# Performance work log

Measured on AMD Instinct MI355X. Metric: run time of the kernel, lower is better.

The kernel has to match this reference:

```python
import jax, jax.numpy as jnp
import numpy as np

N_HEAD = 16

def setup_inputs() -> dict:
    key = jax.random.key(0)
    ks = jax.random.split(key, 5)
    d = 1024
    x = jax.random.normal(ks[0], (2, 2048, d), dtype=jnp.float32)
    Wqkv = jax.random.normal(ks[1], (d, 3 * d), dtype=jnp.float32) * (1.0 / np.sqrt(d))
    bqkv = jnp.zeros((3 * d,), dtype=jnp.float32)
    Wproj = jax.random.normal(ks[2], (d, d), dtype=jnp.float32) * (1.0 / np.sqrt(d))
    bproj = jnp.zeros((d,), dtype=jnp.float32)
    return {"x": x, "Wqkv": Wqkv, "bqkv": bqkv, "Wproj": Wproj, "bproj": bproj}


def reference(x, Wqkv, bqkv, Wproj, bproj):
    B, T, C = x.shape
    H = N_HEAD
    Dh = C // H
    qkv = x @ Wqkv + bqkv                      # [B, T, 3C]
    q, k, v = jnp.split(qkv, 3, axis=-1)
    # [B, T, C] -> [B, H, T, Dh]
    q = q.reshape(B, T, H, Dh).transpose(0, 2, 1, 3)
    k = k.reshape(B, T, H, Dh).transpose(0, 2, 1, 3)
    v = v.reshape(B, T, H, Dh).transpose(0, 2, 1, 3)
    scale = 1.0 / np.sqrt(Dh)
    att = jnp.einsum('bhqd,bhkd->bhqk', q, k) * scale
    causal = jnp.tril(jnp.ones((T, T), dtype=bool))
    att = jnp.where(causal[None, None, :, :], att, jnp.float32(-jnp.inf))
    att = jax.nn.softmax(att, axis=-1)
    y = jnp.einsum('bhqk,bhkd->bhqd', att, v)  # [B, H, T, Dh]
    y = y.transpose(0, 2, 1, 3).reshape(B, T, C)
    return y @ Wproj + bproj
```

## Files before the change

kernel.cpp:

```cpp
#include <hip/hip_runtime.h>
#include <math.h>


typedef __attribute__((ext_vector_type(8))) short short8;
typedef __attribute__((ext_vector_type(4))) short short4v;
typedef __attribute__((ext_vector_type(4))) float floatx4;
typedef __attribute__((ext_vector_type(16))) float floatx16;
typedef __attribute__((ext_vector_type(2))) unsigned int uint2v;
typedef __attribute__((ext_vector_type(4))) unsigned int uint4v;

__device__ __forceinline__ unsigned short f2bf(float f) {
  unsigned u = __float_as_uint(f);
  return (unsigned short)((u + 0x7fff + ((u >> 16) & 1)) >> 16);
}

__device__ __forceinline__ unsigned cvtpk(float a, float b) {
  unsigned r;
  asm("v_cvt_pk_bf16_f32 %0, %1, %2" : "=v"(r) : "v"(a), "v"(b));
  return r;
}

__device__ __forceinline__ short8 mk8(unsigned w0, unsigned w1, unsigned w2,
                                      unsigned w3) {
  uint4v v = {w0, w1, w2, w3};
  return __builtin_bit_cast(short8, v);
}

__device__ __forceinline__ void gld16(const unsigned short* g, unsigned short* l) {
  __builtin_amdgcn_global_load_lds(
      (const __attribute__((address_space(1))) unsigned int*)g,
      (__attribute__((address_space(3))) unsigned int*)l, 16, 0, 0);
}

__device__ __forceinline__ void vmcnt4() {
  asm volatile("s_waitcnt vmcnt(4)" ::: "memory");
}
__device__ __forceinline__ void vmcnt0() {
  asm volatile("s_waitcnt vmcnt(0)" ::: "memory");
}

__device__ __forceinline__ void pack_a_body(const float* __restrict__ in,
                                            unsigned short* __restrict__ out,
                                            int K, int m0, int k0,
                                            unsigned short (*lds)[72], int t) {
  {
    int ml = t >> 2, kl = (t & 3) * 16;
    const float4* p = (const float4*)(in + (size_t)(m0 + ml) * K + k0 + kl);
    unsigned short* q = &lds[ml][kl];
#pragma unroll
    for (int c = 0; c < 4; ++c) {
      float4 v = p[c];
      q[c * 4 + 0] = f2bf(v.x);
      q[c * 4 + 1] = f2bf(v.y);
      q[c * 4 + 2] = f2bf(v.z);
      q[c * 4 + 3] = f2bf(v.w);
    }
  }
  __syncthreads();
  int chunk = t >> 3, sub = t & 7;
  int mt = chunk >> 3, kc = chunk & 7;
  unsigned short tmp[16];
#pragma unroll
  for (int j2 = 0; j2 < 2; ++j2)
#pragma unroll
    for (int j = 0; j < 8; ++j)
      tmp[j2 * 8 + j] = lds[mt * 16 + sub * 2 + j2][kc * 8 + j];
  size_t ofs = ((size_t)(m0 >> 4) + mt) * (16 * (size_t)K) +
               ((size_t)(k0 >> 3) + kc) * 128 + sub * 16;
  *(int4*)(out + ofs) = *(int4*)(tmp);
  *(int4*)(out + ofs + 8) = *(int4*)(tmp + 8);
}

__device__ __forceinline__ void pack_bt_body(const float* __restrict__ in,
                                             unsigned short* __restrict__ out,
                                             int K, int N, int n0, int k0,
                                             unsigned short (*lds)[72], int t) {
  {
    int kl = t >> 2, nl = (t & 3) * 16;
    const float4* p = (const float4*)(in + (size_t)(k0 + kl) * N + n0 + nl);
#pragma unroll
    for (int c = 0; c < 4; ++c) {
      float4 v = p[c];
      lds[nl + c * 4 + 0][kl] = f2bf(v.x);
      lds[nl + c * 4 + 1][kl] = f2bf(v.y);
      lds[nl + c * 4 + 2][kl] = f2bf(v.z);
      lds[nl + c * 4 + 3][kl] = f2bf(v.w);
    }
  }
  __syncthreads();
  int chunk = t >> 3, sub = t & 7;
  int nt = chunk >> 3, kc = chunk & 7;
  unsigned short tmp[16];
#pragma unroll
  for (int j2 = 0; j2 < 2; ++j2)
#pragma unroll
    for (int j = 0; j < 8; ++j)
      tmp[j2 * 8 + j] = lds[nt * 16 + sub * 2 + j2][kc * 8 + j];
  size_t ofs = ((size_t)(n0 >> 4) + nt) * (16 * (size_t)K) +
               ((size_t)(k0 >> 3) + kc) * 128 + sub * 16;
  *(int4*)(out + ofs) = *(int4*)(tmp);
  *(int4*)(out + ofs + 8) = *(int4*)(tmp + 8);
}

__global__ __launch_bounds__(256) void pack_all(
    const float* __restrict__ x, const float* __restrict__ Wqkv,
    const float* __restrict__ Wproj, unsigned short* __restrict__ xbf,
    unsigned short* __restrict__ wqkvF, unsigned short* __restrict__ wprojF) {
  __shared__ __align__(16) unsigned short lds[64][72];
  const int b = blockIdx.x, t = threadIdx.x;
  if (b < 1024) {
    pack_a_body(x, xbf, 1024, (b >> 4) * 64, (b & 15) * 64, lds, t);
  } else if (b < 1792) {
    int b2 = b - 1024;
    pack_bt_body(Wqkv, wqkvF, 1024, 3072, (b2 % 48) * 64, (b2 / 48) * 64, lds, t);
  } else {
    int b3 = b - 1792;
    pack_bt_body(Wproj, wprojF, 1024, 1024, (b3 & 15) * 64, (b3 >> 4) * 64, lds, t);
  }
}

template <int MODE>
__global__ __launch_bounds__(256, 3) void gemm_lds(
    const unsigned short* __restrict__ A, const unsigned short* __restrict__ B,
    const float* __restrict__ bias, float* __restrict__ Cout,
    unsigned short* __restrict__ Qb, unsigned short* __restrict__ Kb,
    unsigned short* __restrict__ Vt, int M, int N, int K) {
  const int tid = threadIdx.x;
  const int wave = tid >> 6, lane = tid & 63;
  const int quad = lane >> 4, l15 = lane & 15;
  const int wr = wave >> 1, wc = wave & 1;

  const int nbn = N >> 7;
  const int colsPerX = nbn >> 3;
  const int xcd = (int)(blockIdx.x & 7);
  const int idx = (int)(blockIdx.x >> 3);
  const int bn = xcd * colsPerX + (colsPerX == 1 ? 0 : (idx % colsPerX));
  const int bm = (colsPerX == 1) ? idx : (idx / colsPerX);

  const int mt0 = bm * 8;
  const int nt0 = bn * 8;

  __shared__ __align__(16) unsigned short As[8192];
  __shared__ __align__(16) unsigned short Bs[8192];

  const unsigned short* spA[4];
  const unsigned short* spB[4];
#pragma unroll
  for (int j = 0; j < 4; ++j) {
    int c = wave * 4 + j;
    spA[j] = A + ((size_t)(mt0 + (c >> 1))) * (16 * (size_t)K) +
             (c & 1) * 512 + lane * 8;
    spB[j] = B + ((size_t)(nt0 + (c >> 1))) * (16 * (size_t)K) +
             (c & 1) * 512 + lane * 8;
  }

  floatx4 acc[4][4];
#pragma unroll
  for (int i = 0; i < 4; ++i)
#pragma unroll
    for (int j = 0; j < 4; ++j) acc[i][j] = (floatx4)0.0f;

  const int fofs = quad * 128 + l15 * 8;
  const int nk = K >> 6;

  for (int kk = 0; kk < nk; ++kk) {
#pragma unroll
    for (int j = 0; j < 4; ++j) {
      gld16(spA[j], &As[(wave * 4 + j) * 512]);
      gld16(spB[j], &Bs[(wave * 4 + j) * 512]);
      spA[j] += 1024;
      spB[j] += 1024;
    }
    __syncthreads();

#pragma unroll
    for (int ks = 0; ks < 2; ++ks) {
      short8 fa[4], fb[4];
#pragma unroll
      for (int im = 0; im < 4; ++im)
        fa[im] = *(const short8*)&As[((wr * 4 + im) * 2 + ks) * 512 + fofs];
#pragma unroll
      for (int in = 0; in < 4; ++in)
        fb[in] = *(const short8*)&Bs[((wc * 4 + in) * 2 + ks) * 512 + fofs];
#pragma unroll
      for (int im = 0; im < 4; ++im)
#pragma unroll
        for (int in = 0; in < 4; ++in)
          acc[im][in] = __builtin_amdgcn_mfma_f32_16x16x32_bf16(
              fa[im], fb[in], acc[im][in], 0, 0, 0);
    }
    if (kk + 1 < nk) __syncthreads();
  }

  const int m0w = bm * 128 + wr * 64;
  const int n0w = bn * 128 + wc * 64;

  if (MODE == 0) {
    const float QSCALE = 0.18033688f;
#pragma unroll
    for (int im = 0; im < 4; ++im) {
      int mbase = m0w + im * 16 + quad * 4;
      int bb = mbase >> 11, tb = mbase & 2047;
#pragma unroll
      for (int in = 0; in < 4; ++in) {
        int n = n0w + in * 16 + l15;
        float bv = bias[n];
        int which = n >> 10;
        int h = (n >> 6) & 15;
        int d = n & 63;
        size_t bh_ = (size_t)(bb * 16 + h);
        if (which == 2) {
          size_t base = bh_ * 131072 + (size_t)(d >> 5) * 65536 +
                        (size_t)(tb >> 4) * 512 +
                        (size_t)((d & 31) + 32 * ((tb & 15) >> 3)) * 8 +
                        (tb & 7);
          short4v pk;
#pragma unroll
          for (int r = 0; r < 4; ++r) pk[r] = (short)f2bf(acc[im][in][r] + bv);
          *(short4v*)(Vt + base) = pk;
        } else {
          size_t base = bh_ * 131072 + (size_t)(tb >> 5) * 2048 +
                        (size_t)(d >> 4) * 512 +
                        (size_t)((tb & 31) + 32 * ((d & 15) >> 3)) * 8 +
                        (d & 7);
          if (which == 0) {
#pragma unroll
            for (int r = 0; r < 4; ++r)
              Qb[base + r * 8] = f2bf((acc[im][in][r] + bv) * QSCALE);
          } else {
#pragma unroll
            for (int r = 0; r < 4; ++r)
              Kb[base + r * 8] = f2bf(acc[im][in][r] + bv);
          }
        }
      }
    }
  } else {
#pragma unroll
    for (int im = 0; im < 4; ++im) {
      int mbase = m0w + im * 16 + quad * 4;
#pragma unroll
      for (int in = 0; in < 4; ++in) {
        int n = n0w + in * 16 + l15;
        float bv = bias[n];
#pragma unroll
        for (int r = 0; r < 4; ++r)
          Cout[(size_t)(mbase + r) * N + n] = acc[im][in][r] + bv;
      }
    }
  }
}

__device__ __forceinline__ void pack_swap(const floatx16& s, short8& lo,
                                          short8& hi) {
  unsigned P0 = cvtpk(s[0], s[1]), P1 = cvtpk(s[2], s[3]);
  unsigned P2 = cvtpk(s[4], s[5]), P3 = cvtpk(s[6], s[7]);
  unsigned P4 = cvtpk(s[8], s[9]), P5 = cvtpk(s[10], s[11]);
  unsigned P6 = cvtpk(s[12], s[13]), P7 = cvtpk(s[14], s[15]);
  uint2v a = __builtin_amdgcn_permlane32_swap(P0, P2, false, false);
  uint2v b = __builtin_amdgcn_permlane32_swap(P1, P3, false, false);
  uint2v c = __builtin_amdgcn_permlane32_swap(P4, P6, false, false);
  uint2v d = __builtin_amdgcn_permlane32_swap(P5, P7, false, false);
  lo = mk8(a.x, b.x, a.y, b.y);
  hi = mk8(c.x, d.x, c.y, d.y);
}

__global__ __launch_bounds__(256, 2) void attn_mfma(
    const unsigned short* __restrict__ Q, const unsigned short* __restrict__ K,
    const unsigned short* __restrict__ Vt, unsigned short* __restrict__ Y) {
  const int b = (int)blockIdx.x;
  const int xcd = b & 7, qi = b >> 3;
  const int bh = xcd * 4 + (qi & 3);
  const int m = 15 - (qi >> 2);
  const int wave = threadIdx.x >> 6;
  const int lane = threadIdx.x & 63;
  const int j = m * 4 + wave;
  const int t0 = j * 32;
  const int l31 = lane & 31, h = lane >> 5;
  const int lofs8 = lane * 8;

  __shared__ __align__(16) unsigned short KV[2][8192];

  const unsigned short* Qb = Q + (size_t)bh * 131072;
  const unsigned short* Kb = K + (size_t)bh * 131072;
  const unsigned short* Vb = Vt + (size_t)bh * 131072;

  auto stage = [&](int buf, int jtN) {
    unsigned short* l = &KV[buf][wave * 2048];
    const unsigned short* g =
        (wave < 2) ? (Kb + (size_t)jtN * 4096 + wave * 2048)
                   : (Vb + (size_t)(wave & 1) * 65536 + (size_t)jtN * 2048);
    g += lofs8;
#pragma unroll
    for (int i = 0; i < 4; ++i) gld16(g + i * 512, l + i * 512);
  };

  short8 qf[4];
#pragma unroll
  for (int c = 0; c < 4; ++c)
    qf[c] = *(const short8*)(Qb + (size_t)j * 2048 + c * 512 + lofs8);

  floatx16 o0 = (floatx16)0.0f, o1 = (floatx16)0.0f;
  float lp[4] = {0.f, 0.f, 0.f, 0.f};

  const int ntiles = (j >> 1) + 1;
  const int ntB = 2 * m + 2;

  stage(0, 0);
  int cur = 0;

  for (int jt = 0; jt < ntB; ++jt) {
    if (jt + 1 < ntB) {
      stage(cur ^ 1, jt + 1);
      vmcnt4();
    } else {
      vmcnt0();
    }
    __builtin_amdgcn_s_barrier();
    __builtin_amdgcn_sched_barrier(0);

    const unsigned short* Lb = KV[cur];
    short8 kf0[4], kf1[4];
#pragma unroll
    for (int c = 0; c < 4; ++c) {
      kf0[c] = *(const short8*)&Lb[c * 512 + lofs8];
      kf1[c] = *(const short8*)&Lb[2048 + c * 512 + lofs8];
    }

    floatx16 sa0 = (floatx16)0.0f, sa1 = (floatx16)0.0f;
#pragma unroll
    for (int c = 0; c < 4; ++c) {
      sa0 = __builtin_amdgcn_mfma_f32_32x32x16_bf16(kf0[c], qf[c], sa0, 0, 0, 0);
      sa1 = __builtin_amdgcn_mfma_f32_32x32x16_bf16(kf1[c], qf[c], sa1, 0, 0, 0);
    }

    if (jt >= ntiles - 1) {
#pragma unroll
      for (int r = 0; r < 16; ++r) {
        int row = (r & 3) + 8 * (r >> 2) + 4 * h;
        int key = jt * 64 + row;
        if (key > t0 + l31) sa0[r] = -__builtin_inff();
        if (key + 32 > t0 + l31) sa1[r] = -__builtin_inff();
      }
    }

#pragma unroll
    for (int r = 0; r < 16; ++r) {
      float p0 = exp2f(sa0[r]);
      float p1 = exp2f(sa1[r]);
      sa0[r] = p0;
      sa1[r] = p1;
      lp[r & 3] += p0 + p1;
    }

    short8 pb0, pb1, pb2, pb3;
    pack_swap(sa0, pb0, pb1);
    pack_swap(sa1, pb2, pb3);

    short8 vf0[4], vf1[4];
#pragma unroll
    for (int kc = 0; kc < 4; ++kc) {
      vf0[kc] = *(const short8*)&Lb[4096 + kc * 512 + lofs8];
      vf1[kc] = *(const short8*)&Lb[6144 + kc * 512 + lofs8];
    }

    o0 = __builtin_amdgcn_mfma_f32_32x32x16_bf16(vf0[0], pb0, o0, 0, 0, 0);
    o1 = __builtin_amdgcn_mfma_f32_32x32x16_bf16(vf1[0], pb0, o1, 0, 0, 0);
    o0 = __builtin_amdgcn_mfma_f32_32x32x16_bf16(vf0[1], pb1, o0, 0, 0, 0);
    o1 = __builtin_amdgcn_mfma_f32_32x32x16_bf16(vf1[1], pb1, o1, 0, 0, 0);
    o0 = __builtin_amdgcn_mfma_f32_32x32x16_bf16(vf0[2], pb2, o0, 0, 0, 0);
    o1 = __builtin_amdgcn_mfma_f32_32x32x16_bf16(vf1[2], pb2, o1, 0, 0, 0);
    o0 = __builtin_amdgcn_mfma_f32_32x32x16_bf16(vf0[3], pb3, o0, 0, 0, 0);
    o1 = __builtin_amdgcn_mfma_f32_32x32x16_bf16(vf1[3], pb3, o1, 0, 0, 0);

    __builtin_amdgcn_sched_barrier(0);
    __builtin_amdgcn_s_barrier();
    cur ^= 1;
  }

  float l_acc = (lp[0] + lp[1]) + (lp[2] + lp[3]);
  l_acc += __shfl_xor(l_acc, 32);
  const float inv = 1.0f / l_acc;

  const int b_ = bh >> 4, hh = bh & 15;
  const int mglob = b_ * 2048 + t0 + l31;
  const size_t mofs = (size_t)(mglob >> 4) * 16384 + (size_t)(mglob & 15) * 8;
#pragma unroll
  for (int db = 0; db < 2; ++db) {
    const floatx16& o = db ? o1 : o0;
#pragma unroll
    for (int g = 0; g < 4; ++g) {
      int d0 = db * 32 + 8 * g + 4 * h;
      int kf0 = hh * 64 + d0;
      size_t ofs = mofs + (size_t)(kf0 >> 3) * 128 + (kf0 & 7);
      short4v pk;
#pragma unroll
      for (int r = 0; r < 4; ++r) pk[r] = (short)f2bf(o[4 * g + r] * inv);
      *(short4v*)(Y + ofs) = pk;
    }
  }
}

extern "C" void kernel_launch(void* const* d_in, const int* in_sizes, int n_in,
                              void* d_out, int out_size, void* d_ws,
                              size_t ws_size, hipStream_t stream) {
  const float* x = (const float*)d_in[0];
  const float* Wqkv = (const float*)d_in[1];
  const float* bqkv = (const float*)d_in[2];
  const float* Wproj = (const float*)d_in[3];
  const float* bproj = (const float*)d_in[4];
  float* out = (float*)d_out;

  const int C = 1024;
  const int M = 4096;

  char* ws = (char*)d_ws;
  unsigned short* qbuf = (unsigned short*)ws;
  unsigned short* kbuf = (unsigned short*)(ws + 8388608);
  unsigned short* vtbuf = (unsigned short*)(ws + 16777216);
  unsigned short* ybuf = (unsigned short*)(ws + 25165824);
  unsigned short* xbf = (unsigned short*)(ws + 33554432);
  unsigned short* wqkvF = (unsigned short*)(ws + 41943040);
  unsigned short* wprojF = (unsigned short*)(ws + 48234496);

  dim3 blk(256);
  pack_all<<<dim3(2048), blk, 0, stream>>>(x, Wqkv, Wproj, xbf, wqkvF, wprojF);
  gemm_lds<0><<<dim3((M / 128) * (3 * C / 128)), blk, 0, stream>>>(
      xbf, wqkvF, bqkv, nullptr, qbuf, kbuf, vtbuf, M, 3 * C, C);
  attn_mfma<<<dim3(512), blk, 0, stream>>>(qbuf, kbuf, vtbuf, ybuf);
  gemm_lds<1><<<dim3((M / 128) * (C / 128)), blk, 0, stream>>>(
      ybuf, wprojF, bproj, out, nullptr, nullptr, nullptr, M, C, C);
}
```

Before: 178.7 us.

## Double-buffer GEMM LDS tiles with vmcnt waits and reorder attention block scheduling

The GEMM main loop moves from a single 64-wide K tile with two full syncthreads per iteration to a double-buffered 32-wide K pipeline. Two stages are prefetched up front, and each iteration waits with vmcnt on the older loads, so global-to-LDS copies overlap the MFMA work. The attention kernel's block-to-query-tile mapping changes so the first 256 blocks take the heavy causal tiles in descending order and the rest take the light tiles in ascending order, to balance work across waves of blocks. The cost is twice as many barriers per unit of K and reliance on exact vmcnt counts for correctness.

```diff
diff --git a/kernel.cpp b/kernel.cpp
--- a/kernel.cpp
+++ b/kernel.cpp
@@ -140,18 +140,15 @@
   const int mt0 = bm * 8;
   const int nt0 = bn * 8;
 
-  __shared__ __align__(16) unsigned short As[8192];
-  __shared__ __align__(16) unsigned short Bs[8192];
-
-  const unsigned short* spA[4];
-  const unsigned short* spB[4];
-#pragma unroll
-  for (int j = 0; j < 4; ++j) {
-    int c = wave * 4 + j;
-    spA[j] = A + ((size_t)(mt0 + (c >> 1))) * (16 * (size_t)K) +
-             (c & 1) * 512 + lane * 8;
-    spB[j] = B + ((size_t)(nt0 + (c >> 1))) * (16 * (size_t)K) +
-             (c & 1) * 512 + lane * 8;
+  __shared__ __align__(16) unsigned short As[2][4096];
+  __shared__ __align__(16) unsigned short Bs[2][4096];
+
+  const unsigned short* spA[2];
+  const unsigned short* spB[2];
+#pragma unroll
+  for (int jj = 0; jj < 2; ++jj) {
+    spA[jj] = A + ((size_t)(mt0 + wave * 2 + jj)) * (16 * (size_t)K) + lane * 8;
+    spB[jj] = B + ((size_t)(nt0 + wave * 2 + jj)) * (16 * (size_t)K) + lane * 8;
   }
 
   floatx4 acc[4][4];
@@ -161,35 +158,56 @@
     for (int j = 0; j < 4; ++j) acc[i][j] = (floatx4)0.0f;
 
   const int fofs = quad * 128 + l15 * 8;
-  const int nk = K >> 6;
+  const int nk = K >> 5;
+
+#pragma unroll
+  for (int jj = 0; jj < 2; ++jj) {
+    gld16(spA[jj], &As[0][(wave * 2 + jj) * 512]);
+    gld16(spB[jj], &Bs[0][(wave * 2 + jj) * 512]);
+    spA[jj] += 512;
+    spB[jj] += 512;
+  }
+#pragma unroll
+  for (int jj = 0; jj < 2; ++jj) {
+    gld16(spA[jj], &As[1][(wave * 2 + jj) * 512]);
+    gld16(spB[jj], &Bs[1][(wave * 2 + jj) * 512]);
+    spA[jj] += 512;
+    spB[jj] += 512;
+  }
 
   for (int kk = 0; kk < nk; ++kk) {
-#pragma unroll
-    for (int j = 0; j < 4; ++j) {
-      gld16(spA[j], &As[(wave * 4 + j) * 512]);
-      gld16(spB[j], &Bs[(wave * 4 + j) * 512]);
-      spA[j] += 1024;
-      spB[j] += 1024;
-    }
-    __syncthreads();
-
-#pragma unroll
-    for (int ks = 0; ks < 2; ++ks) {
-      short8 fa[4], fb[4];
-#pragma unroll
-      for (int im = 0; im < 4; ++im)
-        fa[im] = *(const short8*)&As[((wr * 4 + im) * 2 + ks) * 512 + fofs];
+    if (kk + 1 < nk) vmcnt4(); else vmcnt0();
+    __builtin_amdgcn_s_barrier();
+    __builtin_amdgcn_sched_barrier(0);
+
+    const unsigned short* Ab = As[kk & 1];
+    const unsigned short* Bb = Bs[kk & 1];
+    short8 fa[4], fb[4];
+#pragma unroll
+    for (int im = 0; im < 4; ++im)
+      fa[im] = *(const short8*)&Ab[(wr * 4 + im) * 512 + fofs];
+#pragma unroll
+    for (int in = 0; in < 4; ++in)
+      fb[in] = *(const short8*)&Bb[(wc * 4 + in) * 512 + fofs];
+#pragma unroll
+    for (int im = 0; im < 4; ++im)
 #pragma unroll
       for (int in = 0; in < 4; ++in)
-        fb[in] = *(const short8*)&Bs[((wc * 4 + in) * 2 + ks) * 512 + fofs];
-#pragma unroll
-      for (int im = 0; im < 4; ++im)
-#pragma unroll
-        for (int in = 0; in < 4; ++in)
-          acc[im][in] = __builtin_amdgcn_mfma_f32_16x16x32_bf16(
-              fa[im], fb[in], acc[im][in], 0, 0, 0);
-    }
-    if (kk + 1 < nk) __syncthreads();
+        acc[im][in] = __builtin_amdgcn_mfma_f32_16x16x32_bf16(
+            fa[im], fb[in], acc[im][in], 0, 0, 0);
+
+    __builtin_amdgcn_sched_barrier(0);
+    __builtin_amdgcn_s_barrier();
+
+    if (kk + 2 < nk) {
+#pragma unroll
+      for (int jj = 0; jj < 2; ++jj) {
+        gld16(spA[jj], &As[kk & 1][(wave * 2 + jj) * 512]);
+        gld16(spB[jj], &Bs[kk & 1][(wave * 2 + jj) * 512]);
+        spA[jj] += 512;
+        spB[jj] += 512;
+      }
+    }
   }
 
   const int m0w = bm * 128 + wr * 64;
@@ -269,9 +287,10 @@
     const unsigned short* __restrict__ Q, const unsigned short* __restrict__ K,
     const unsigned short* __restrict__ Vt, unsigned short* __restrict__ Y) {
   const int b = (int)blockIdx.x;
-  const int xcd = b & 7, qi = b >> 3;
-  const int bh = xcd * 4 + (qi & 3);
-  const int m = 15 - (qi >> 2);
+  const int xcd = b & 7;
+  const int bh = xcd * 4 + ((b >> 3) & 3);
+  const int k = (b >> 5) & 7;
+  const int m = (b < 256) ? (15 - k) : k;
   const int wave = threadIdx.x >> 6;
   const int lane = threadIdx.x & 63;
   const int j = m * 4 + wave;
```

Result: no change. 180.4 us (+1.0%).
